# Performance work log

Measured on AMD Instinct MI355X. Metric: run time of the kernel, lower is better.

Reference implementation:

```python
import jax, jax.numpy as jnp
import numpy as np

B, N, IN_DIM, H, D = 4, 2048, 128, 4, 64
NEG_SLOPE = 0.2
MASK_VAL = -1e9


def setup_inputs() -> dict:
    key = jax.random.key(0)
    k1, k2, k3, k4, k5 = jax.random.split(key, 5)
    x = jax.random.normal(k1, (B, N, IN_DIM), dtype=jnp.float32)
    adj = jax.random.randint(k2, (N, N), 0, 2, dtype=jnp.int32)
    W = jax.random.normal(k3, (H * D, IN_DIM), dtype=jnp.float32) * 0.05
    att_src = jax.random.normal(k4, (1, H, D), dtype=jnp.float32) * 0.05
    att_dst = jax.random.normal(k5, (1, H, D), dtype=jnp.float32) * 0.05
    return {"x": x, "adj": adj, "W": W, "att_src": att_src, "att_dst": att_dst}


def reference(x, adj, W, att_src, att_dst):
    # linear (no bias), torch layout: y = x @ W.T  -> [B,N,H*D]
    h = jnp.einsum('bni,oi->bno', x, W).reshape(B, N, H, D).transpose(0, 2, 1, 3)  # [B,H,N,D]
    e_src = jnp.einsum('bhnd,hd->bhn', h, att_src[0])  # [B,H,N]
    e_dst = jnp.einsum('bhnd,hd->bhn', h, att_dst[0])  # [B,H,N]
    # additive score: e[b,h,i,j] = leaky_relu(e_src[b,h,i] + e_dst[b,h,j])
    e = jax.nn.leaky_relu(e_src[..., :, None] + e_dst[..., None, :], NEG_SLOPE)  # [B,H,N,N]
    e = jnp.where(adj[None, None] <= 0, MASK_VAL, e)
    attn = jax.nn.softmax(e, axis=-1)  # dropout inactive (inference)
    out = jnp.einsum('bhij,bhjd->bhid', attn, h)  # [B,H,N,D]
    return out.transpose(0, 2, 1, 3).reshape(B, N, H * D)  # concat heads
```

## Files before the change

kernel.cpp:

```cpp
#include <hip/hip_runtime.h>


#define NDIM 2048
#define NEG_SLOPE 0.2f

typedef __bf16 bf16x8 __attribute__((ext_vector_type(8)));
typedef __bf16 bf16x4 __attribute__((ext_vector_type(4)));
typedef float  f32x4  __attribute__((ext_vector_type(4)));

#define LPITCH 136
#define APITCH 72

__global__ __launch_bounds__(256) void adj_pack(const int* __restrict__ adj,
                                                unsigned* __restrict__ bits) {
    const int t = threadIdx.x;
    const int q = blockIdx.x * 256 + t;
    int4 a = ((const int4*)adj)[q];
    unsigned nib = (unsigned)(a.x > 0) | ((unsigned)(a.y > 0) << 1) |
                   ((unsigned)(a.z > 0) << 2) | ((unsigned)(a.w > 0) << 3);
    unsigned v = nib << ((t & 7) * 4);
    v |= __shfl_xor(v, 1, 64);
    v |= __shfl_xor(v, 2, 64);
    v |= __shfl_xor(v, 4, 64);
    if ((t & 7) == 0) bits[q >> 3] = v;
}

__global__ __launch_bounds__(256) void gat_linear(
    const float* __restrict__ x, const float* __restrict__ W,
    const float* __restrict__ att_src, const float* __restrict__ att_dst,
    __bf16* __restrict__ h_t, float* __restrict__ es_ws, float* __restrict__ ed_ws)
{
    const int t    = threadIdx.x;
    const int blk  = blockIdx.x;
    const int chh  = blk & 1;
    const int row0 = (blk >> 1) * 32;
    const int b    = row0 >> 11;
    const int n0   = row0 & (NDIM - 1);

    __shared__ __align__(16) __bf16 Wl[128][LPITCH];
    __shared__ __align__(16) __bf16 Xl[32][LPITCH];

    #pragma unroll 4
    for (int i = 0; i < 16; ++i) {
        int idx = t + i * 256;
        int r = idx >> 5, c4 = idx & 31;
        float4 wv = *((const float4*)(W + (size_t)(chh * 128 + r) * 128) + c4);
        bf16x4 bv;
        bv[0] = (__bf16)wv.x; bv[1] = (__bf16)wv.y; bv[2] = (__bf16)wv.z; bv[3] = (__bf16)wv.w;
        *(bf16x4*)&Wl[r][c4 * 4] = bv;
    }
    #pragma unroll
    for (int i = 0; i < 4; ++i) {
        int idx = t + i * 256;
        int r = idx >> 5, c4 = idx & 31;
        float4 xv = *((const float4*)(x + (size_t)(row0 + r) * 128) + c4);
        bf16x4 bv;
        bv[0] = (__bf16)xv.x; bv[1] = (__bf16)xv.y; bv[2] = (__bf16)xv.z; bv[3] = (__bf16)xv.w;
        *(bf16x4*)&Xl[r][c4 * 4] = bv;
    }
    __syncthreads();

    const int lane = t & 63, w = t >> 6;
    const int m = lane & 15, q = lane >> 4;
    const int rt = w & 1;
    const int cb = (w >> 1) * 4;

    bf16x8 af[4];
    #pragma unroll
    for (int ks = 0; ks < 4; ++ks)
        af[ks] = *(const bf16x8*)&Xl[rt * 16 + m][ks * 32 + q * 8];

    f32x4 acc[4];
    #pragma unroll
    for (int c = 0; c < 4; ++c) acc[c] = (f32x4){0.f, 0.f, 0.f, 0.f};

    #pragma unroll
    for (int c = 0; c < 4; ++c) {
        const int ct = cb + c;
        #pragma unroll
        for (int ks = 0; ks < 4; ++ks) {
            bf16x8 bfr = *(const bf16x8*)&Wl[ct * 16 + m][ks * 32 + q * 8];
            acc[c] = __builtin_amdgcn_mfma_f32_16x16x32_bf16(af[ks], bfr, acc[c], 0, 0, 0);
        }
    }

    const int hh = chh * 2 + (w >> 1);
    const int bh = b * 4 + hh;
    float esA[4] = {0.f, 0.f, 0.f, 0.f}, edA[4] = {0.f, 0.f, 0.f, 0.f};
    #pragma unroll
    for (int c = 0; c < 4; ++c) {
        const int ct   = cb + c;
        const int colg = chh * 128 + ct * 16 + m;
        const int d    = colg & 63;
        const float aS = att_src[colg], aD = att_dst[colg];
        bf16x4 hv;
        #pragma unroll
        for (int r = 0; r < 4; ++r) {
            float v = acc[c][r];
            hv[r] = (__bf16)v;
            esA[r] += v * aS;
            edA[r] += v * aD;
        }
        *(bf16x4*)(h_t + (size_t)(bh * 64 + d) * NDIM + n0 + rt * 16 + q * 4) = hv;
    }
    #pragma unroll
    for (int off = 1; off < 16; off <<= 1) {
        #pragma unroll
        for (int r = 0; r < 4; ++r) {
            esA[r] += __shfl_xor(esA[r], off, 64);
            edA[r] += __shfl_xor(edA[r], off, 64);
        }
    }
    if (m == 0) {
        #pragma unroll
        for (int r = 0; r < 4; ++r) {
            int n = n0 + rt * 16 + q * 4 + r;
            es_ws[bh * NDIM + n] = esA[r];
            ed_ws[bh * NDIM + n] = edA[r];
        }
    }
}

__global__ __launch_bounds__(256) void gat_attn(
    const unsigned* __restrict__ bits, const __bf16* __restrict__ h_t,
    const float* __restrict__ es_ws, const float* __restrict__ ed_ws,
    float* __restrict__ out)
{
    const int blk = blockIdx.x;
    const int bh  = blk >> 5;
    const int i0  = (blk & 31) * 64;
    const int t   = threadIdx.x;
    const int lane = t & 63, w = t >> 6;
    const int m = lane & 15, q = lane >> 4;

    __shared__ __align__(16) __bf16 Pl[64][APITCH];
    __shared__ __align__(16) __bf16 Hl[64][APITCH];
    __shared__ float eds[NDIM];
    __shared__ float ess[64];
    __shared__ float lred[4][64];
    __shared__ float linv[64];

    {
        const float4* src = (const float4*)(ed_ws + bh * NDIM);
        ((float4*)eds)[t]       = src[t];
        ((float4*)eds)[t + 256] = src[t + 256];
    }
    if (t < 64) ess[t] = es_ws[bh * NDIM + i0 + t];
    __syncthreads();

    const int il = t >> 2;
    const int ch = t & 3;
    const float es_i = ess[il];
    const unsigned* brow = bits + (size_t)(i0 + il) * 64;
    const __bf16*   hrow = h_t + (size_t)(bh * 64 + il) * NDIM;

    f32x4 acc[4];
    #pragma unroll
    for (int c = 0; c < 4; ++c) acc[c] = (f32x4){0.f, 0.f, 0.f, 0.f};
    float lacc = 0.f;

    for (int j0 = 0; j0 < NDIM; j0 += 64) {
        {
            const __bf16* gp = hrow + j0 + ch * 16;
            *(bf16x8*)&Hl[il][ch * 16]     = *(const bf16x8*)gp;
            *(bf16x8*)&Hl[il][ch * 16 + 8] = *(const bf16x8*)(gp + 8);
        }
        {
            unsigned word = brow[(j0 >> 5) + (ch >> 1)];
            unsigned bm = (word >> ((ch & 1) * 16)) & 0xFFFFu;
            float ev[16];
            #pragma unroll
            for (int g = 0; g < 4; ++g)
                *(float4*)&ev[g * 4] = *(const float4*)(eds + j0 + ch * 16 + g * 4);
            float pv[16];
            #pragma unroll
            for (int jj = 0; jj < 16; ++jj) {
                float s = es_i + ev[jj];
                s = fmaxf(s, NEG_SLOPE * s);
                float e = __expf(s);
                float p = ((bm >> jj) & 1u) ? e : 0.f;
                pv[jj] = p;
                lacc += p;
            }
            bf16x8 v0, v1;
            #pragma unroll
            for (int jj = 0; jj < 8; ++jj) { v0[jj] = (__bf16)pv[jj]; v1[jj] = (__bf16)pv[jj + 8]; }
            *(bf16x8*)&Pl[il][ch * 16]     = v0;
            *(bf16x8*)&Pl[il][ch * 16 + 8] = v1;
        }
        __syncthreads();

        #pragma unroll
        for (int ks = 0; ks < 2; ++ks) {
            bf16x8 a = *(const bf16x8*)&Pl[w * 16 + m][ks * 32 + q * 8];
            #pragma unroll
            for (int ct = 0; ct < 4; ++ct) {
                bf16x8 bfr = *(const bf16x8*)&Hl[ct * 16 + m][ks * 32 + q * 8];
                acc[ct] = __builtin_amdgcn_mfma_f32_16x16x32_bf16(a, bfr, acc[ct], 0, 0, 0);
            }
        }
        __syncthreads();
    }

    lred[ch][il] = lacc;
    __syncthreads();
    if (t < 64) linv[t] = 1.f / (lred[0][t] + lred[1][t] + lred[2][t] + lred[3][t]);
    __syncthreads();

    const int b_ = bh >> 2, hh = bh & 3;
    float* obase = out + ((size_t)b_ * NDIM + i0) * 256 + hh * 64;
    #pragma unroll
    for (int ct = 0; ct < 4; ++ct) {
        #pragma unroll
        for (int r = 0; r < 4; ++r) {
            int row = w * 16 + q * 4 + r;
            obase[(size_t)row * 256 + ct * 16 + m] = acc[ct][r] * linv[row];
        }
    }
}

extern "C" void kernel_launch(void* const* d_in, const int* in_sizes, int n_in,
                              void* d_out, int out_size, void* d_ws, size_t ws_size,
                              hipStream_t stream) {
    const float* x       = (const float*)d_in[0];
    const int*   adj     = (const int*)d_in[1];
    const float* W       = (const float*)d_in[2];
    const float* att_src = (const float*)d_in[3];
    const float* att_dst = (const float*)d_in[4];
    float* out = (float*)d_out;

    __bf16*   h_t   = (__bf16*)d_ws;
    float*    es_ws = (float*)((char*)d_ws + (size_t)4 * 1024 * 1024);
    float*    ed_ws = es_ws + 16 * NDIM;
    unsigned* bitsp = (unsigned*)(ed_ws + 16 * NDIM);

    adj_pack<<<NDIM * NDIM / 4 / 256, 256, 0, stream>>>(adj, bitsp);
    gat_linear<<<512, 256, 0, stream>>>(x, W, att_src, att_dst, h_t, es_ws, ed_ws);
    gat_attn<<<512, 256, 0, stream>>>(bitsp, h_t, es_ws, ed_ws, out);
}
```

Measured before the change: 114.7 us.

## Compute softmax probabilities in registers and double-buffer H tiles in attention

The attention kernel now builds the probability fragments directly in MFMA A-operand registers instead of staging them through shared memory. It uses exp2 with log2e-prescaled scores and double-buffers the H tile, prefetching the next tile while the current one is consumed, which leaves one barrier per iteration. Row sums are reduced with shuffles, and block order is changed so heads interleave. The linear kernel is reorganized to one head per block with a transposed MFMA mapping. The trade-off is scalar 2-byte h_t stores and higher register use.

```diff
diff --git a/kernel.cpp b/kernel.cpp
--- a/kernel.cpp
+++ b/kernel.cpp
@@ -3,13 +3,14 @@
 
 #define NDIM 2048
 #define NEG_SLOPE 0.2f
+#define LOG2E 1.4426950408889634f
 
 typedef __bf16 bf16x8 __attribute__((ext_vector_type(8)));
 typedef __bf16 bf16x4 __attribute__((ext_vector_type(4)));
 typedef float  f32x4  __attribute__((ext_vector_type(4)));
 
-#define LPITCH 136
-#define APITCH 72
+#define LP 136
+#define HP 72
 
 __global__ __launch_bounds__(256) void adj_pack(const int* __restrict__ adj,
                                                 unsigned* __restrict__ bits) {
@@ -31,29 +32,29 @@
     __bf16* __restrict__ h_t, float* __restrict__ es_ws, float* __restrict__ ed_ws)
 {
     const int t    = threadIdx.x;
-    const int blk  = blockIdx.x;
-    const int chh  = blk & 1;
-    const int row0 = (blk >> 1) * 32;
-    const int b    = row0 >> 11;
-    const int n0   = row0 & (NDIM - 1);
-
-    __shared__ __align__(16) __bf16 Wl[128][LPITCH];
-    __shared__ __align__(16) __bf16 Xl[32][LPITCH];
-
-    #pragma unroll 4
-    for (int i = 0; i < 16; ++i) {
+    const int head = blockIdx.x & 3;
+    const int n0g  = (blockIdx.x >> 2) * 64;
+    const int b    = n0g >> 11;
+    const int n0   = n0g & (NDIM - 1);
+    const int bh   = b * 4 + head;
+
+    __shared__ __align__(16) __bf16 Wl[64][LP];
+    __shared__ __align__(16) __bf16 Xl[64][LP];
+
+    #pragma unroll
+    for (int i = 0; i < 8; ++i) {
         int idx = t + i * 256;
         int r = idx >> 5, c4 = idx & 31;
-        float4 wv = *((const float4*)(W + (size_t)(chh * 128 + r) * 128) + c4);
+        float4 wv = *((const float4*)(W + (size_t)(head * 64 + r) * 128) + c4);
         bf16x4 bv;
         bv[0] = (__bf16)wv.x; bv[1] = (__bf16)wv.y; bv[2] = (__bf16)wv.z; bv[3] = (__bf16)wv.w;
         *(bf16x4*)&Wl[r][c4 * 4] = bv;
     }
     #pragma unroll
-    for (int i = 0; i < 4; ++i) {
+    for (int i = 0; i < 8; ++i) {
         int idx = t + i * 256;
         int r = idx >> 5, c4 = idx & 31;
-        float4 xv = *((const float4*)(x + (size_t)(row0 + r) * 128) + c4);
+        float4 xv = *((const float4*)(x + (size_t)(n0g + r) * 128) + c4);
         bf16x4 bv;
         bv[0] = (__bf16)xv.x; bv[1] = (__bf16)xv.y; bv[2] = (__bf16)xv.z; bv[3] = (__bf16)xv.w;
         *(bf16x4*)&Xl[r][c4 * 4] = bv;
@@ -61,160 +62,150 @@
     __syncthreads();
 
     const int lane = t & 63, w = t >> 6;
-    const int m = lane & 15, q = lane >> 4;
-    const int rt = w & 1;
-    const int cb = (w >> 1) * 4;
-
-    bf16x8 af[4];
+    const int m = lane & 15, q4 = lane >> 4;
+
+    bf16x8 bfr[4];
     #pragma unroll
     for (int ks = 0; ks < 4; ++ks)
-        af[ks] = *(const bf16x8*)&Xl[rt * 16 + m][ks * 32 + q * 8];
+        bfr[ks] = *(const bf16x8*)&Xl[w * 16 + m][ks * 32 + q4 * 8];
 
     f32x4 acc[4];
     #pragma unroll
     for (int c = 0; c < 4; ++c) acc[c] = (f32x4){0.f, 0.f, 0.f, 0.f};
 
     #pragma unroll
-    for (int c = 0; c < 4; ++c) {
-        const int ct = cb + c;
+    for (int ct = 0; ct < 4; ++ct) {
         #pragma unroll
         for (int ks = 0; ks < 4; ++ks) {
-            bf16x8 bfr = *(const bf16x8*)&Wl[ct * 16 + m][ks * 32 + q * 8];
-            acc[c] = __builtin_amdgcn_mfma_f32_16x16x32_bf16(af[ks], bfr, acc[c], 0, 0, 0);
-        }
-    }
-
-    const int hh = chh * 2 + (w >> 1);
-    const int bh = b * 4 + hh;
-    float esA[4] = {0.f, 0.f, 0.f, 0.f}, edA[4] = {0.f, 0.f, 0.f, 0.f};
-    #pragma unroll
-    for (int c = 0; c < 4; ++c) {
-        const int ct   = cb + c;
-        const int colg = chh * 128 + ct * 16 + m;
-        const int d    = colg & 63;
-        const float aS = att_src[colg], aD = att_dst[colg];
-        bf16x4 hv;
+            bf16x8 afr = *(const bf16x8*)&Wl[ct * 16 + m][ks * 32 + q4 * 8];
+            acc[ct] = __builtin_amdgcn_mfma_f32_16x16x32_bf16(afr, bfr[ks], acc[ct], 0, 0, 0);
+        }
+    }
+
+    const int nloc = n0 + w * 16 + m;
+    float esA = 0.f, edA = 0.f;
+    #pragma unroll
+    for (int ct = 0; ct < 4; ++ct) {
+        float4 aS = *(const float4*)(att_src + head * 64 + ct * 16 + q4 * 4);
+        float4 aD = *(const float4*)(att_dst + head * 64 + ct * 16 + q4 * 4);
         #pragma unroll
         for (int r = 0; r < 4; ++r) {
-            float v = acc[c][r];
-            hv[r] = (__bf16)v;
-            esA[r] += v * aS;
-            edA[r] += v * aD;
-        }
-        *(bf16x4*)(h_t + (size_t)(bh * 64 + d) * NDIM + n0 + rt * 16 + q * 4) = hv;
-    }
-    #pragma unroll
-    for (int off = 1; off < 16; off <<= 1) {
-        #pragma unroll
-        for (int r = 0; r < 4; ++r) {
-            esA[r] += __shfl_xor(esA[r], off, 64);
-            edA[r] += __shfl_xor(edA[r], off, 64);
-        }
-    }
-    if (m == 0) {
-        #pragma unroll
-        for (int r = 0; r < 4; ++r) {
-            int n = n0 + rt * 16 + q * 4 + r;
-            es_ws[bh * NDIM + n] = esA[r];
-            ed_ws[bh * NDIM + n] = edA[r];
-        }
+            float v = acc[ct][r];
+            int   d = ct * 16 + q4 * 4 + r;
+            h_t[(size_t)(bh * 64 + d) * NDIM + nloc] = (__bf16)v;
+            esA += v * ((const float*)&aS)[r];
+            edA += v * ((const float*)&aD)[r];
+        }
+    }
+    esA += __shfl_xor(esA, 16, 64); esA += __shfl_xor(esA, 32, 64);
+    edA += __shfl_xor(edA, 16, 64); edA += __shfl_xor(edA, 32, 64);
+    if (lane < 16) {
+        es_ws[bh * NDIM + nloc] = esA;
+        ed_ws[bh * NDIM + nloc] = edA;
     }
 }
 
 __global__ __launch_bounds__(256) void gat_attn(
-    const unsigned* __restrict__ bits, const __bf16* __restrict__ h_t,
+    const unsigned long long* __restrict__ bits, const __bf16* __restrict__ h_t,
     const float* __restrict__ es_ws, const float* __restrict__ ed_ws,
     float* __restrict__ out)
 {
     const int blk = blockIdx.x;
-    const int bh  = blk >> 5;
-    const int i0  = (blk & 31) * 64;
+    const int bh  = blk & 15;
+    const int i0  = (blk >> 4) * 64;
     const int t   = threadIdx.x;
     const int lane = t & 63, w = t >> 6;
-    const int m = lane & 15, q = lane >> 4;
-
-    __shared__ __align__(16) __bf16 Pl[64][APITCH];
-    __shared__ __align__(16) __bf16 Hl[64][APITCH];
-    __shared__ float eds[NDIM];
-    __shared__ float ess[64];
-    __shared__ float lred[4][64];
-    __shared__ float linv[64];
-
-    {
-        const float4* src = (const float4*)(ed_ws + bh * NDIM);
-        ((float4*)eds)[t]       = src[t];
-        ((float4*)eds)[t + 256] = src[t + 256];
-    }
-    if (t < 64) ess[t] = es_ws[bh * NDIM + i0 + t];
-    __syncthreads();
-
+    const int m = lane & 15, q4 = lane >> 4;
     const int il = t >> 2;
     const int ch = t & 3;
-    const float es_i = ess[il];
-    const unsigned* brow = bits + (size_t)(i0 + il) * 64;
-    const __bf16*   hrow = h_t + (size_t)(bh * 64 + il) * NDIM;
+
+    __shared__ __align__(16) __bf16 Hl[2][64][HP];
+    __shared__ float eds[NDIM];
+
+    #pragma unroll
+    for (int k = 0; k < 2; ++k) {
+        int idx = t + k * 256;
+        float4 v = ((const float4*)(ed_ws + bh * NDIM))[idx];
+        v.x *= LOG2E; v.y *= LOG2E; v.z *= LOG2E; v.w *= LOG2E;
+        ((float4*)eds)[idx] = v;
+    }
+    const float es2 = es_ws[bh * NDIM + i0 + w * 16 + m] * LOG2E;
+    const unsigned long long* brow = bits + (size_t)(i0 + w * 16 + m) * 32;
+
+    const __bf16* hbase = h_t + (size_t)(bh * 64 + il) * NDIM + ch * 16;
+    {
+        bf16x8 c0 = *(const bf16x8*)hbase;
+        bf16x8 c1 = *(const bf16x8*)(hbase + 8);
+        *(bf16x8*)&Hl[0][il][ch * 16]     = c0;
+        *(bf16x8*)&Hl[0][il][ch * 16 + 8] = c1;
+    }
+    __syncthreads();
 
     f32x4 acc[4];
     #pragma unroll
     for (int c = 0; c < 4; ++c) acc[c] = (f32x4){0.f, 0.f, 0.f, 0.f};
     float lacc = 0.f;
 
-    for (int j0 = 0; j0 < NDIM; j0 += 64) {
-        {
-            const __bf16* gp = hrow + j0 + ch * 16;
-            *(bf16x8*)&Hl[il][ch * 16]     = *(const bf16x8*)gp;
-            *(bf16x8*)&Hl[il][ch * 16 + 8] = *(const bf16x8*)(gp + 8);
-        }
-        {
-            unsigned word = brow[(j0 >> 5) + (ch >> 1)];
-            unsigned bm = (word >> ((ch & 1) * 16)) & 0xFFFFu;
-            float ev[16];
+    for (int itj = 0; itj < 32; ++itj) {
+        const int buf = itj & 1;
+        const bool hn = itj < 31;
+        bf16x8 n0v, n1v;
+        if (hn) {
+            const __bf16* gp = hbase + (itj + 1) * 64;
+            n0v = *(const bf16x8*)gp;
+            n1v = *(const bf16x8*)(gp + 8);
+        }
+
+        const unsigned long long bw = brow[itj];
+        const int j0 = itj * 64;
+        bf16x8 af[2];
+        #pragma unroll
+        for (int ks = 0; ks < 2; ++ks) {
+            float e[8];
+            *(float4*)&e[0] = *(const float4*)&eds[j0 + ks * 32 + q4 * 8];
+            *(float4*)&e[4] = *(const float4*)&eds[j0 + ks * 32 + q4 * 8 + 4];
+            unsigned bm = (unsigned)(bw >> (ks * 32 + q4 * 8)) & 0xFFu;
             #pragma unroll
-            for (int g = 0; g < 4; ++g)
-                *(float4*)&ev[g * 4] = *(const float4*)(eds + j0 + ch * 16 + g * 4);
-            float pv[16];
-            #pragma unroll
-            for (int jj = 0; jj < 16; ++jj) {
-                float s = es_i + ev[jj];
+            for (int jj = 0; jj < 8; ++jj) {
+                float s = es2 + e[jj];
                 s = fmaxf(s, NEG_SLOPE * s);
-                float e = __expf(s);
-                float p = ((bm >> jj) & 1u) ? e : 0.f;
-                pv[jj] = p;
+                s = ((bm >> jj) & 1u) ? s : -10000.0f;
+                float p = __builtin_amdgcn_exp2f(s);
                 lacc += p;
+                af[ks][jj] = (__bf16)p;
             }
-            bf16x8 v0, v1;
-            #pragma unroll
-            for (int jj = 0; jj < 8; ++jj) { v0[jj] = (__bf16)pv[jj]; v1[jj] = (__bf16)pv[jj + 8]; }
-            *(bf16x8*)&Pl[il][ch * 16]     = v0;
-            *(bf16x8*)&Pl[il][ch * 16 + 8] = v1;
-        }
-        __syncthreads();
+        }
 
         #pragma unroll
         for (int ks = 0; ks < 2; ++ks) {
-            bf16x8 a = *(const bf16x8*)&Pl[w * 16 + m][ks * 32 + q * 8];
             #pragma unroll
             for (int ct = 0; ct < 4; ++ct) {
-                bf16x8 bfr = *(const bf16x8*)&Hl[ct * 16 + m][ks * 32 + q * 8];
-                acc[ct] = __builtin_amdgcn_mfma_f32_16x16x32_bf16(a, bfr, acc[ct], 0, 0, 0);
+                bf16x8 bfr = *(const bf16x8*)&Hl[buf][ct * 16 + m][ks * 32 + q4 * 8];
+                acc[ct] = __builtin_amdgcn_mfma_f32_16x16x32_bf16(af[ks], bfr, acc[ct], 0, 0, 0);
             }
         }
+
+        if (hn) {
+            *(bf16x8*)&Hl[buf ^ 1][il][ch * 16]     = n0v;
+            *(bf16x8*)&Hl[buf ^ 1][il][ch * 16 + 8] = n1v;
+        }
         __syncthreads();
     }
 
-    lred[ch][il] = lacc;
-    __syncthreads();
-    if (t < 64) linv[t] = 1.f / (lred[0][t] + lred[1][t] + lred[2][t] + lred[3][t]);
-    __syncthreads();
-
-    const int b_ = bh >> 2, hh = bh & 3;
-    float* obase = out + ((size_t)b_ * NDIM + i0) * 256 + hh * 64;
+    lacc += __shfl_xor(lacc, 16, 64);
+    lacc += __shfl_xor(lacc, 32, 64);
+    const float inv = 1.f / lacc;
+    float invr[4];
+    #pragma unroll
+    for (int r = 0; r < 4; ++r) invr[r] = __shfl(inv, q4 * 4 + r, 64);
+
+    const int b = bh >> 2, head = bh & 3;
+    float* ob = out + ((size_t)(b * NDIM + i0 + w * 16)) * 256 + head * 64;
     #pragma unroll
     for (int ct = 0; ct < 4; ++ct) {
         #pragma unroll
         for (int r = 0; r < 4; ++r) {
-            int row = w * 16 + q * 4 + r;
-            obase[(size_t)row * 256 + ct * 16 + m] = acc[ct][r] * linv[row];
+            ob[(size_t)(q4 * 4 + r) * 256 + ct * 16 + m] = acc[ct][r] * invr[r];
         }
     }
 }
@@ -236,5 +227,5 @@
 
     adj_pack<<<NDIM * NDIM / 4 / 256, 256, 0, stream>>>(adj, bitsp);
     gat_linear<<<512, 256, 0, stream>>>(x, W, att_src, att_dst, h_t, es_ws, ed_ws);
-    gat_attn<<<512, 256, 0, stream>>>(bitsp, h_t, es_ws, ed_ws, out);
-}
+    gat_attn<<<512, 256, 0, stream>>>((const unsigned long long*)bitsp, h_t, es_ws, ed_ws, out);
+}
```

Result: faster. 108.6 us (-5.3%).
